# Kernel tuning notes

Measured on AMD Instinct MI355X. Metric: run time of the kernel, lower is better.

Reference implementation:

```python
import jax, jax.numpy as jnp
import numpy as np

GAMMA = 0.95  # usage decay from NTM.__init__

def setup_inputs() -> dict:
    key = jax.random.key(0)
    ks = jax.random.split(key, 16)
    B, N, M, R, U, Din = 256, 32768, 64, 4, 256, 512
    Dc = Din + R * M  # controller input = x concat prev read vectors
    s = 0.02
    x = jax.random.normal(ks[0], (B, Din), jnp.float32)
    A = jax.random.normal(ks[1], (N, M), jnp.float32) * 0.1
    wr_prev = jax.nn.softmax(jax.random.normal(ks[2], (R, B, N), jnp.float32), axis=-1)
    wu_prev = jax.random.uniform(ks[3], (B, N), jnp.float32)
    read_prev = jax.random.normal(ks[4], (R, B, M), jnp.float32) * 0.1
    h = jax.random.normal(ks[5], (B, U), jnp.float32) * 0.1
    c = jax.random.normal(ks[6], (B, U), jnp.float32) * 0.1
    W = jax.random.normal(ks[7], (Dc, 4 * U), jnp.float32) * s
    Uw = jax.random.normal(ks[8], (U, 4 * U), jnp.float32) * s
    b = jnp.zeros((4 * U,), jnp.float32)
    Wk = jax.random.normal(ks[9], (R, U, M), jnp.float32) * s
    bk = jnp.zeros((R, M), jnp.float32)
    Wa = jax.random.normal(ks[10], (U, R), jnp.float32) * s
    ba = jnp.zeros((R,), jnp.float32)
    return dict(x=x, A=A, wr_prev=wr_prev, wu_prev=wu_prev, read_prev=read_prev,
                h=h, c=c, W=W, Uw=Uw, b=b, Wk=Wk, bk=bk, Wa=Wa, ba=ba)

def reference(x, A, wr_prev, wu_prev, read_prev, h, c, W, Uw, b, Wk, bk, Wa, ba):
    B, N = wu_prev.shape
    R, _, M = read_prev.shape
    # ---- controller (single LSTM cell step, keras gate order i,f,g,o) ----
    ctrl_in = jnp.concatenate([x, read_prev.transpose(1, 0, 2).reshape(B, -1)], axis=-1)
    gates = ctrl_in @ W + h @ Uw + b
    gi, gf, gg, go = jnp.split(gates, 4, axis=-1)
    c_new = jax.nn.sigmoid(gf) * c + jax.nn.sigmoid(gi) * jnp.tanh(gg)
    h_new = jax.nn.sigmoid(go) * jnp.tanh(c_new)  # controller_output [B,U]
    # ---- least-used weights from previous usage ----
    least = jnp.argmin(wu_prev, axis=-1)                       # [B]
    wlu = jax.nn.one_hot(least, N, dtype=wu_prev.dtype)        # [B,N]
    # ---- read heads: cosine-similarity content addressing ----
    kt = jnp.tanh(jnp.einsum('bu,rum->rbm', h_new, Wk) + bk[:, None, :])  # [R,B,M]
    inner = jnp.einsum('rbm,nm->rbn', kt, A)                   # [R,B,N]
    knorm = jnp.linalg.norm(kt, axis=-1)                       # [R,B]
    anorm = jnp.linalg.norm(A, axis=-1)                        # [N]
    Ksim = inner / (knorm[..., None] * anorm[None, None, :] + 1e-16)
    wr = jax.nn.softmax(Ksim, axis=-1)                         # [R,B,N]
    # ---- write head: gated mix of prev read weights and least-used ----
    alpha = jax.nn.sigmoid(jnp.tanh(h_new @ Wa + ba))          # [B,R]
    a = alpha.T[:, :, None]                                    # [R,B,1]
    ww = a * wr_prev + (1.0 - a) * wlu[None]                   # [R,B,N]
    # ---- usage update ----
    wu = GAMMA * wu_prev + jnp.sum(wr + ww, axis=0)            # [B,N]
    # ---- memory: erase least-used row(s), then tanh additive writes ----
    erase = 1.0 - jnp.max(wlu, axis=0)                         # [N]
    A_new = A * erase[:, None]
    for r in range(R):  # small fixed head count
        A_new = jnp.tanh(A_new + jnp.einsum('bn,bm->nm', ww[r], kt[r]))
    # ---- reads and output ----
    reads = jnp.einsum('rbn,nm->rbm', wr, A_new)               # [R,B,M]
    out = jnp.concatenate([h_new, reads.transpose(1, 0, 2).reshape(B, -1)], axis=-1)
    return out
```

## Files before the change

### kernel.cpp

```cpp
#include <hip/hip_runtime.h>
#include <hip/hip_bf16.h>
#include <stdint.h>

#define B_   256
#define N_   32768
#define M_   64
#define R_   4
#define U_   256
#define DIN_ 512
#define DC_  768
#define J4_  1024
#define Q_   1024

__device__ __forceinline__ float sigm(float x){ return 1.f/(1.f+__expf(-x)); }
__device__ __forceinline__ float tanh_f(float x){ float e=__expf(2.f*x); return 1.f - 2.f/(e+1.f); }
__device__ __forceinline__ unsigned short f2bf(float x){
    unsigned u = __float_as_uint(x);
    u += 0x7FFFu + ((u>>16)&1u);
    return (unsigned short)(u>>16);
}
__device__ __forceinline__ float bflo(unsigned u){ return __uint_as_float(u << 16); }
__device__ __forceinline__ float bfhi(unsigned u){ return __uint_as_float(u & 0xFFFF0000u); }

__global__ __launch_bounds__(256) void k_zero(int* lflag, float* l){
    int i = blockIdx.x*256 + threadIdx.x;
    if(i < N_) lflag[i] = 0;
    if(i < Q_) l[i] = 0.f;
}

__global__ __launch_bounds__(256) void k_anorm(const float* A, float* anorm){
    int n = blockIdx.x*4 + (threadIdx.x>>6);
    int lane = threadIdx.x & 63;
    float v = A[n*64 + lane];
    float s = v*v;
    #pragma unroll
    for(int m=1;m<64;m<<=1) s += __shfl_xor(s, m, 64);
    if(lane==0) anorm[n] = sqrtf(s);
}

__global__ __launch_bounds__(256) void k_argmin(const float* wu, int* least, int* lflag){
    __shared__ float sv[256]; __shared__ int si[256];
    int b = blockIdx.x, t = threadIdx.x;
    const float* row = wu + (size_t)b*N_;
    float bv = 3.4e38f; int bi = 0;
    for(int n=t; n<N_; n+=256){ float v = row[n]; if(v < bv){ bv=v; bi=n; } }
    sv[t]=bv; si[t]=bi; __syncthreads();
    for(int s=128;s>0;s>>=1){
        if(t<s){
            float ov=sv[t+s]; int oi=si[t+s];
            if(ov<sv[t] || (ov==sv[t] && oi<si[t])){ sv[t]=ov; si[t]=oi; }
        }
        __syncthreads();
    }
    if(t==0){ least[b]=si[0]; lflag[si[0]]=1; }
}

__global__ __launch_bounds__(256) void k_lstm_gemm(const float* x, const float* rp, const float* h,
                                                   const float* W, const float* Uw, float* gpart){
    __shared__ float s_in[8*128];
    int bt = blockIdx.x >> 3, ks = blockIdx.x & 7;
    int b0 = bt*8, t = threadIdx.x;
    for(int i=t; i<1024; i+=256){
        int bb = i>>7, kk = i&127, k = ks*128 + kk, b = b0+bb;
        float v;
        if(k < DIN_) v = x[b*DIN_ + k];
        else if(k < DC_){ int k2 = k - DIN_; v = rp[(k2>>6)*(B_*M_) + b*M_ + (k2&63)]; }
        else v = h[b*U_ + (k-DC_)];
        s_in[bb*128 + kk] = v;
    }
    __syncthreads();
    float4 acc[8];
    #pragma unroll
    for(int i=0;i<8;i++) acc[i] = make_float4(0.f,0.f,0.f,0.f);
    const float* Wsel; int krel;
    if(ks < 6){ Wsel = W; krel = ks*128; } else { Wsel = Uw; krel = ks*128 - DC_; }
    int j0 = t*4;
    for(int kk=0; kk<128; kk++){
        float4 w = *(const float4*)(Wsel + (size_t)(krel+kk)*J4_ + j0);
        #pragma unroll
        for(int bb=0;bb<8;bb++){
            float s = s_in[bb*128 + kk];
            acc[bb].x += s*w.x; acc[bb].y += s*w.y; acc[bb].z += s*w.z; acc[bb].w += s*w.w;
        }
    }
    #pragma unroll
    for(int bb=0;bb<8;bb++)
        *(float4*)(gpart + (size_t)ks*(B_*J4_) + (size_t)(b0+bb)*J4_ + j0) = acc[bb];
}

__global__ __launch_bounds__(256) void k_lstm_act(const float* gpart, const float* bias, const float* c,
                                                  float* h_new, float* out){
    int b = blockIdx.x, u = threadIdx.x;
    float gi=bias[u], gf=bias[256+u], gg=bias[512+u], go=bias[768+u];
    #pragma unroll
    for(int s=0;s<8;s++){
        const float* gp = gpart + (size_t)s*(B_*J4_) + (size_t)b*J4_;
        gi += gp[u]; gf += gp[256+u]; gg += gp[512+u]; go += gp[768+u];
    }
    float cn = sigm(gf)*c[b*U_+u] + sigm(gi)*tanh_f(gg);
    float hn = sigm(go)*tanh_f(cn);
    h_new[b*U_+u] = hn;
    out[(size_t)b*512 + u] = hn;
}

__global__ __launch_bounds__(64) void k_kta(const float* h_new, const float* Wk, const float* bk,
                                            const float* Wa, const float* ba,
                                            float* kt, float* aktw, float* alpha, float* knorm){
    __shared__ float h_l[256];
    int r = blockIdx.x >> 8, b = blockIdx.x & 255, m = threadIdx.x;
    for(int i=m;i<256;i+=64) h_l[i] = h_new[b*U_ + i];
    __syncthreads();
    float acc = bk[r*64 + m];
    const float* wkp = Wk + (size_t)r*U_*M_ + m;
    for(int u=0;u<256;u++) acc += h_l[u] * wkp[u*64];
    float k = tanh_f(acc);
    float s = k*k;
    #pragma unroll
    for(int mm=1;mm<64;mm<<=1) s += __shfl_xor(s, mm, 64);
    float pa = 0.f;
    #pragma unroll
    for(int uu=0; uu<4; uu++){ int u = m*4+uu; pa += h_l[u]*Wa[u*R_ + r]; }
    #pragma unroll
    for(int mm=1;mm<64;mm<<=1) pa += __shfl_xor(pa, mm, 64);
    float al = sigm(tanh_f(pa + ba[r]));
    int q = r*256 + b;
    kt[q*64 + m]   = k;
    aktw[q*64 + m] = al*k;
    if(m==0){ knorm[q] = sqrtf(s); alpha[q] = al; }
}

__global__ __launch_bounds__(256,2) void k_Ggemm(const float* wrp, const float* aktw, float* G){
    __shared__ float wr_l[32*256];
    __shared__ float akt_l[32*64];
    int r = blockIdx.x >> 7, nt = blockIdx.x & 127;
    int nb = nt*256, t = threadIdx.x;
    int tm = t & 15, tn = t >> 4;
    const float* wbase = wrp  + (size_t)r*((size_t)B_*N_);
    const float* abase = aktw + (size_t)r*(B_*M_);
    float4 acc[16];
    #pragma unroll
    for(int i=0;i<16;i++) acc[i]=make_float4(0.f,0.f,0.f,0.f);
    for(int tile=0; tile<8; tile++){
        int bb0 = tile*32;
        __syncthreads();
        for(int i=t; i<2048; i+=256){
            int kk = i>>6, cc = i&63;
            *(float4*)(wr_l + kk*256 + cc*4) = *(const float4*)(wbase + (size_t)(bb0+kk)*N_ + nb + cc*4);
        }
        for(int i=t; i<512; i+=256){
            int kk = i>>4, cc = i&15;
            *(float4*)(akt_l + kk*64 + cc*4) = *(const float4*)(abase + (bb0+kk)*64 + cc*4);
        }
        __syncthreads();
        #pragma unroll 4
        for(int kk=0; kk<32; kk++){
            float4 af = *(const float4*)(akt_l + kk*64 + tm*4);
            float4 w0 = *(const float4*)(wr_l + kk*256 + tn*16);
            float4 w1 = *(const float4*)(wr_l + kk*256 + tn*16 + 4);
            float4 w2 = *(const float4*)(wr_l + kk*256 + tn*16 + 8);
            float4 w3 = *(const float4*)(wr_l + kk*256 + tn*16 + 12);
#define GFMA(I, WV) { acc[I].x += (WV)*af.x; acc[I].y += (WV)*af.y; acc[I].z += (WV)*af.z; acc[I].w += (WV)*af.w; }
            GFMA(0,w0.x) GFMA(1,w0.y) GFMA(2,w0.z) GFMA(3,w0.w)
            GFMA(4,w1.x) GFMA(5,w1.y) GFMA(6,w1.z) GFMA(7,w1.w)
            GFMA(8,w2.x) GFMA(9,w2.y) GFMA(10,w2.z) GFMA(11,w2.w)
            GFMA(12,w3.x) GFMA(13,w3.y) GFMA(14,w3.z) GFMA(15,w3.w)
#undef GFMA
        }
    }
    float* gout = G + (size_t)r*((size_t)N_*64);
    #pragma unroll
    for(int i=0;i<16;i++)
        *(float4*)(gout + (size_t)(nb + tn*16 + i)*64 + tm*4) = acc[i];
}

__global__ __launch_bounds__(64) void k_scatter(const float* kt, const float* alpha, const int* least, float* G){
    int r = blockIdx.x >> 8, b = blockIdx.x & 255, m = threadIdx.x;
    int q = r*256+b;
    float v = (1.f - alpha[q]) * kt[q*64 + m];
    int row = least[b];
    atomicAdd(G + (size_t)r*((size_t)N_*64) + (size_t)row*64 + m, v);
}

__global__ __launch_bounds__(256) void k_Aupd(const float* A, const float* G, const int* lflag, float* Anew){
    int i4 = blockIdx.x*256 + threadIdx.x;
    int n = i4 >> 4;
    float er = lflag[n] ? 0.f : 1.f;
    float4 a = ((const float4*)A)[i4];
    float4 v = make_float4(a.x*er, a.y*er, a.z*er, a.w*er);
    #pragma unroll
    for(int r=0;r<4;r++){
        float4 g = ((const float4*)G)[(size_t)r*524288 + i4];
        v.x = tanh_f(v.x+g.x); v.y = tanh_f(v.y+g.y); v.z = tanh_f(v.z+g.z); v.w = tanh_f(v.w+g.w);
    }
    ((float4*)Anew)[i4] = v;
}

__global__ __launch_bounds__(256,2) void k_scores(const float* kt, const float* A,
                                                  const float* knorm, const float* anorm,
                                                  unsigned short* Pt, float* l){
    __shared__ float4 kt_l[128*16];
    __shared__ float4 A_l[128*16];
    int nt = blockIdx.x >> 3, qt = blockIdx.x & 7;
    int nb = nt*128, qb = qt*128;
    int t = threadIdx.x, tq = t & 15, tn = t >> 4;
    for(int i=t;i<2048;i+=256){
        int row = i>>4, cc = i&15;
        kt_l[row*16 + (cc ^ (row>>3))] = *(const float4*)(kt + (qb+row)*64 + cc*4);
        A_l [row*16 + (cc ^ (row>>3))] = *(const float4*)(A + (size_t)(nb+row)*64 + cc*4);
    }
    __syncthreads();
    float acc[64];
    #pragma unroll
    for(int i=0;i<64;i++) acc[i]=0.f;
    #pragma unroll
    for(int mq=0; mq<16; mq++){
        float4 kf[8], af[8];
        #pragma unroll
        for(int i=0;i<8;i++) kf[i] = kt_l[(tq*8+i)*16 + (mq ^ tq)];
        #pragma unroll
        for(int j=0;j<8;j++) af[j] = A_l[(tn*8+j)*16 + (mq ^ tn)];
        #pragma unroll
        for(int i=0;i<8;i++)
        #pragma unroll
        for(int j=0;j<8;j++)
            acc[i*8+j] += kf[i].x*af[j].x + kf[i].y*af[j].y + kf[i].z*af[j].z + kf[i].w*af[j].w;
    }
    float kn[8], an[8];
    #pragma unroll
    for(int i=0;i<8;i++) kn[i] = knorm[qb + tq*8 + i];
    #pragma unroll
    for(int j=0;j<8;j++) an[j] = anorm[nb + tn*8 + j];
    float lp[8];
    #pragma unroll
    for(int i=0;i<8;i++) lp[i]=0.f;
    #pragma unroll
    for(int j=0;j<8;j++){
        unsigned pk[4];
        #pragma unroll
        for(int i2=0;i2<4;i2++){
            float p0 = __expf(__fdividef(acc[(i2*2  )*8+j], kn[i2*2  ]*an[j] + 1e-16f));
            float p1 = __expf(__fdividef(acc[(i2*2+1)*8+j], kn[i2*2+1]*an[j] + 1e-16f));
            lp[i2*2] += p0; lp[i2*2+1] += p1;
            pk[i2] = (unsigned)f2bf(p0) | ((unsigned)f2bf(p1)<<16);
        }
        *(uint4*)(Pt + (size_t)(nb + tn*8 + j)*Q_ + qb + tq*8) = make_uint4(pk[0],pk[1],pk[2],pk[3]);
    }
    __syncthreads();
    float* lred = (float*)A_l;
    #pragma unroll
    for(int i=0;i<8;i++) lred[tn*128 + tq*8 + i] = lp[i];
    __syncthreads();
    if(t < 128){
        float s = 0.f;
        #pragma unroll
        for(int g=0; g<16; g++) s += lred[g*128 + t];
        atomicAdd(l + qb + t, s);
    }
}

__global__ __launch_bounds__(256,4) void k_pv(const unsigned short* Pt, const float* Anew, float* part){
    __shared__ uint4  P_l[32*16];
    __shared__ float4 V_l[32*16];
    int ch = blockIdx.x >> 3, qt = blockIdx.x & 7;
    int qb = qt*128, n0c = ch*512;
    int t = threadIdx.x, tq = t & 15, tm = t >> 4;
    float4 acc[8];
    #pragma unroll
    for(int i=0;i<8;i++) acc[i]=make_float4(0.f,0.f,0.f,0.f);
    for(int tile=0; tile<16; tile++){
        int n0 = n0c + tile*32;
        __syncthreads();
        for(int i=t;i<512;i+=256){
            int row = i>>4, cc = i&15;
            P_l[row*16 + cc] = *(const uint4*)(Pt + (size_t)(n0+row)*Q_ + qb + cc*8);
            V_l[row*16 + cc] = *(const float4*)(Anew + (size_t)(n0+row)*64 + cc*4);
        }
        __syncthreads();
        #pragma unroll 4
        for(int kk=0;kk<32;kk++){
            uint4 pw = P_l[kk*16 + tq];
            float4 vf = V_l[kk*16 + tm];
            float p0=bflo(pw.x), p1=bfhi(pw.x), p2=bflo(pw.y), p3=bfhi(pw.y);
            float p4=bflo(pw.z), p5=bfhi(pw.z), p6=bflo(pw.w), p7=bfhi(pw.w);
#define PVF(I, PV) { acc[I].x += (PV)*vf.x; acc[I].y += (PV)*vf.y; acc[I].z += (PV)*vf.z; acc[I].w += (PV)*vf.w; }
            PVF(0,p0) PVF(1,p1) PVF(2,p2) PVF(3,p3) PVF(4,p4) PVF(5,p5) PVF(6,p6) PVF(7,p7)
#undef PVF
        }
    }
    #pragma unroll
    for(int i=0;i<8;i++)
        *(float4*)(part + (size_t)ch*(Q_*64) + (size_t)(qb + tq*8 + i)*64 + tm*4) = acc[i];
}

__global__ __launch_bounds__(256) void k_reduce(const float* part, const float* l, float* out){
    int tg = blockIdx.x*256 + threadIdx.x;
    int q = tg >> 6, m = tg & 63;
    float s = 0.f;
    for(int cc=0;cc<64;cc++) s += part[(size_t)cc*(Q_*64) + tg];
    float val = s / l[q];
    int r = q >> 8, b = q & 255;
    out[(size_t)b*512 + 256 + r*64 + m] = val;
}

extern "C" void kernel_launch(void* const* d_in, const int* in_sizes, int n_in,
                              void* d_out, int out_size, void* d_ws, size_t ws_size,
                              hipStream_t stream) {
    const float* x        = (const float*)d_in[0];
    const float* A        = (const float*)d_in[1];
    const float* wr_prev  = (const float*)d_in[2];
    const float* wu_prev  = (const float*)d_in[3];
    const float* read_prev= (const float*)d_in[4];
    const float* h        = (const float*)d_in[5];
    const float* c        = (const float*)d_in[6];
    const float* W        = (const float*)d_in[7];
    const float* Uw       = (const float*)d_in[8];
    const float* bvec     = (const float*)d_in[9];
    const float* Wk       = (const float*)d_in[10];
    const float* bk       = (const float*)d_in[11];
    const float* Wa       = (const float*)d_in[12];
    const float* ba       = (const float*)d_in[13];
    float* out = (float*)d_out;

    char* wsp = (char*)d_ws;
    float* G      = (float*)(wsp);
    float* Anew   = (float*)(wsp + 33554432);
    unsigned short* Pt = (unsigned short*)(wsp + 41943040);
    float* h_new  = (float*)(wsp + 109051904);
    float* kt     = (float*)(wsp + 109314048);
    float* aktw   = (float*)(wsp + 109576192);
    float* alpha  = (float*)(wsp + 109838336);
    float* knorm  = (float*)(wsp + 109842432);
    float* anorm  = (float*)(wsp + 109846528);
    int*   lflag  = (int*)  (wsp + 109977600);
    float* l      = (float*)(wsp + 110108672);
    int*   least  = (int*)  (wsp + 110112768);

    k_zero     <<<128, 256, 0, stream>>>(lflag, l);
    k_anorm    <<<8192,256, 0, stream>>>(A, anorm);
    k_argmin   <<<256, 256, 0, stream>>>(wu_prev, least, lflag);
    k_lstm_gemm<<<256, 256, 0, stream>>>(x, read_prev, h, W, Uw, G);
    k_lstm_act <<<256, 256, 0, stream>>>(G, bvec, c, h_new, out);
    k_kta      <<<1024, 64, 0, stream>>>(h_new, Wk, bk, Wa, ba, kt, aktw, alpha, knorm);
    k_Ggemm    <<<512, 256, 0, stream>>>(wr_prev, aktw, G);
    k_scatter  <<<1024, 64, 0, stream>>>(kt, alpha, least, G);
    k_Aupd     <<<2048,256, 0, stream>>>(A, G, lflag, Anew);
    k_scores   <<<2048,256, 0, stream>>>(kt, A, knorm, anorm, Pt, l);
    k_pv       <<<512, 256, 0, stream>>>(Pt, Anew, G);
    k_reduce   <<<256, 256, 0, stream>>>(G, l, out);
}
```

Before: 558.2 us.

## Fuse scores and PV into flash-style bf16 MFMA attention kernel

Result: faster. 494.9 us (-11.3%).

```diff
diff --git a/kernel.cpp b/kernel.cpp
--- a/kernel.cpp
+++ b/kernel.cpp
@@ -11,6 +11,10 @@
 #define DC_  768
 #define J4_  1024
 #define Q_   1024
+#define NPART_ 32
+
+typedef __attribute__((ext_vector_type(8))) short short8v;
+typedef __attribute__((ext_vector_type(4))) float f32x4;
 
 __device__ __forceinline__ float sigm(float x){ return 1.f/(1.f+__expf(-x)); }
 __device__ __forceinline__ float tanh_f(float x){ float e=__expf(2.f*x); return 1.f - 2.f/(e+1.f); }
@@ -19,8 +23,6 @@
     u += 0x7FFFu + ((u>>16)&1u);
     return (unsigned short)(u>>16);
 }
-__device__ __forceinline__ float bflo(unsigned u){ return __uint_as_float(u << 16); }
-__device__ __forceinline__ float bfhi(unsigned u){ return __uint_as_float(u & 0xFFFF0000u); }
 
 __global__ __launch_bounds__(256) void k_zero(int* lflag, float* l){
     int i = blockIdx.x*256 + threadIdx.x;
@@ -28,10 +30,11 @@
     if(i < Q_) l[i] = 0.f;
 }
 
-__global__ __launch_bounds__(256) void k_anorm(const float* A, float* anorm){
+__global__ __launch_bounds__(256) void k_anorm(const float* A, float* anorm, unsigned short* A_bf){
     int n = blockIdx.x*4 + (threadIdx.x>>6);
     int lane = threadIdx.x & 63;
     float v = A[n*64 + lane];
+    A_bf[n*64 + lane] = f2bf(v);
     float s = v*v;
     #pragma unroll
     for(int m=1;m<64;m<<=1) s += __shfl_xor(s, m, 64);
@@ -105,7 +108,8 @@
 
 __global__ __launch_bounds__(64) void k_kta(const float* h_new, const float* Wk, const float* bk,
                                             const float* Wa, const float* ba,
-                                            float* kt, float* aktw, float* alpha, float* knorm){
+                                            float* kt, unsigned short* kt_bf, float* aktw,
+                                            float* alpha, float* knorm){
     __shared__ float h_l[256];
     int r = blockIdx.x >> 8, b = blockIdx.x & 255, m = threadIdx.x;
     for(int i=m;i<256;i+=64) h_l[i] = h_new[b*U_ + i];
@@ -124,8 +128,9 @@
     for(int mm=1;mm<64;mm<<=1) pa += __shfl_xor(pa, mm, 64);
     float al = sigm(tanh_f(pa + ba[r]));
     int q = r*256 + b;
-    kt[q*64 + m]   = k;
-    aktw[q*64 + m] = al*k;
+    kt[q*64 + m]    = k;
+    kt_bf[q*64 + m] = f2bf(k);
+    aktw[q*64 + m]  = al*k;
     if(m==0){ knorm[q] = sqrtf(s); alpha[q] = al; }
 }
 
@@ -195,108 +200,107 @@
     ((float4*)Anew)[i4] = v;
 }
 
-__global__ __launch_bounds__(256,2) void k_scores(const float* kt, const float* A,
-                                                  const float* knorm, const float* anorm,
-                                                  unsigned short* Pt, float* l){
-    __shared__ float4 kt_l[128*16];
-    __shared__ float4 A_l[128*16];
-    int nt = blockIdx.x >> 3, qt = blockIdx.x & 7;
-    int nb = nt*128, qb = qt*128;
-    int t = threadIdx.x, tq = t & 15, tn = t >> 4;
-    for(int i=t;i<2048;i+=256){
-        int row = i>>4, cc = i&15;
-        kt_l[row*16 + (cc ^ (row>>3))] = *(const float4*)(kt + (qb+row)*64 + cc*4);
-        A_l [row*16 + (cc ^ (row>>3))] = *(const float4*)(A + (size_t)(nb+row)*64 + cc*4);
+__global__ __launch_bounds__(256) void k_vt(const float* Anew, unsigned short* Vt){
+    __shared__ __align__(16) unsigned short lt[4096];
+    int n0 = blockIdx.x*64, t = threadIdx.x;
+    int row = t>>2, cb = t&3;
+    #pragma unroll
+    for(int i=0;i<4;i++){
+        int cidx = cb*4 + i;
+        float4 f = *(const float4*)(Anew + (size_t)(n0+row)*64 + cidx*4);
+        int m0 = cidx*4;
+        lt[(m0  )*64 + row] = f2bf(f.x);
+        lt[(m0+1)*64 + row] = f2bf(f.y);
+        lt[(m0+2)*64 + row] = f2bf(f.z);
+        lt[(m0+3)*64 + row] = f2bf(f.w);
     }
     __syncthreads();
-    float acc[64];
-    #pragma unroll
-    for(int i=0;i<64;i++) acc[i]=0.f;
-    #pragma unroll
-    for(int mq=0; mq<16; mq++){
-        float4 kf[8], af[8];
+    int mr = t>>2;
+    #pragma unroll
+    for(int cc=0; cc<2; cc++){
+        int c = (t&3) + cc*4;
+        uint4 v = *(const uint4*)(lt + mr*64 + c*8);
+        *(uint4*)(Vt + (size_t)mr*N_ + n0 + c*8) = v;
+    }
+}
+
+__global__ __launch_bounds__(256) void k_attn(const unsigned short* kt_bf, const unsigned short* A_bf,
+                                              const unsigned short* Vt, const float* knorm,
+                                              const float* anorm, float* part, float* l){
+    __shared__ __align__(16) unsigned short Pl[64*256];
+    int nc = blockIdx.x >> 4, qt = blockIdx.x & 15;
+    int qb = qt*64, nb = nc*1024;
+    int lane = threadIdx.x & 63, w = threadIdx.x >> 6;
+    int r16 = lane & 15, hq = lane >> 4;
+    const short8v* kp = (const short8v*)(kt_bf + (size_t)(qb + w*16 + r16)*64 + hq*8);
+    short8v ka0 = kp[0], ka1 = kp[4];
+    float kn[4];
+    #pragma unroll
+    for(int j=0;j<4;j++) kn[j] = knorm[qb + w*16 + hq*4 + j];
+    f32x4 O[4];
+    #pragma unroll
+    for(int mt=0;mt<4;mt++) O[mt] = (f32x4){0.f,0.f,0.f,0.f};
+    float lp[4] = {0.f,0.f,0.f,0.f};
+    int g2 = (r16 >> 2) & 3;
+
+    for(int c=0; c<4; c++){
+        int n0c = nb + c*256;
+        __syncthreads();
+        for(int nt=0; nt<16; nt++){
+            int ntb = n0c + nt*16;
+            const short8v* bp = (const short8v*)(A_bf + (size_t)(ntb + r16)*64 + hq*8);
+            f32x4 acc = (f32x4){0.f,0.f,0.f,0.f};
+            acc = __builtin_amdgcn_mfma_f32_16x16x32_bf16(ka0, bp[0], acc, 0, 0, 0);
+            acc = __builtin_amdgcn_mfma_f32_16x16x32_bf16(ka1, bp[4], acc, 0, 0, 0);
+            float an = anorm[ntb + r16];
+            unsigned um[4];
+            #pragma unroll
+            for(int j=0;j<4;j++){
+                float p = __expf(__fdividef(acc[j], kn[j]*an + 1e-16f));
+                lp[j] += p;
+                um[j] = (unsigned)f2bf(p);
+            }
+            int nl = nt*16 + (r16 & ~1);
+            #pragma unroll
+            for(int j=0;j<4;j++){
+                unsigned up = __shfl_xor((int)um[j], 1, 64);
+                if((lane & 1) == 0){
+                    unsigned word = um[j] | (up << 16);
+                    int byteoff = (w*16 + hq*4 + j)*512 + ((nl ^ (hq<<4)) << 1);
+                    *(unsigned*)((char*)Pl + byteoff) = word;
+                }
+            }
+        }
+        __syncthreads();
+        #pragma unroll 2
+        for(int ks=0; ks<8; ks++){
+            short8v pa = *(const short8v*)((const char*)Pl +
+                          ((w*16 + r16)*512 + (((ks*32 + hq*8) ^ (g2<<4)) << 1)));
+            #pragma unroll
+            for(int mt=0; mt<4; mt++){
+                const short8v* vp = (const short8v*)(Vt + (size_t)(mt*16 + r16)*N_ + n0c + ks*32 + hq*8);
+                O[mt] = __builtin_amdgcn_mfma_f32_16x16x32_bf16(pa, vp[0], O[mt], 0, 0, 0);
+            }
+        }
+    }
+    #pragma unroll
+    for(int mt=0; mt<4; mt++)
         #pragma unroll
-        for(int i=0;i<8;i++) kf[i] = kt_l[(tq*8+i)*16 + (mq ^ tq)];
+        for(int j=0;j<4;j++)
+            part[((size_t)nc*Q_ + (qb + w*16 + hq*4 + j))*64 + mt*16 + r16] = O[mt][j];
+    #pragma unroll
+    for(int j=0;j<4;j++){
         #pragma unroll
-        for(int j=0;j<8;j++) af[j] = A_l[(tn*8+j)*16 + (mq ^ tn)];
-        #pragma unroll
-        for(int i=0;i<8;i++)
-        #pragma unroll
-        for(int j=0;j<8;j++)
-            acc[i*8+j] += kf[i].x*af[j].x + kf[i].y*af[j].y + kf[i].z*af[j].z + kf[i].w*af[j].w;
-    }
-    float kn[8], an[8];
-    #pragma unroll
-    for(int i=0;i<8;i++) kn[i] = knorm[qb + tq*8 + i];
-    #pragma unroll
-    for(int j=0;j<8;j++) an[j] = anorm[nb + tn*8 + j];
-    float lp[8];
-    #pragma unroll
-    for(int i=0;i<8;i++) lp[i]=0.f;
-    #pragma unroll
-    for(int j=0;j<8;j++){
-        unsigned pk[4];
-        #pragma unroll
-        for(int i2=0;i2<4;i2++){
-            float p0 = __expf(__fdividef(acc[(i2*2  )*8+j], kn[i2*2  ]*an[j] + 1e-16f));
-            float p1 = __expf(__fdividef(acc[(i2*2+1)*8+j], kn[i2*2+1]*an[j] + 1e-16f));
-            lp[i2*2] += p0; lp[i2*2+1] += p1;
-            pk[i2] = (unsigned)f2bf(p0) | ((unsigned)f2bf(p1)<<16);
-        }
-        *(uint4*)(Pt + (size_t)(nb + tn*8 + j)*Q_ + qb + tq*8) = make_uint4(pk[0],pk[1],pk[2],pk[3]);
-    }
-    __syncthreads();
-    float* lred = (float*)A_l;
-    #pragma unroll
-    for(int i=0;i<8;i++) lred[tn*128 + tq*8 + i] = lp[i];
-    __syncthreads();
-    if(t < 128){
-        float s = 0.f;
-        #pragma unroll
-        for(int g=0; g<16; g++) s += lred[g*128 + t];
-        atomicAdd(l + qb + t, s);
-    }
-}
-
-__global__ __launch_bounds__(256,4) void k_pv(const unsigned short* Pt, const float* Anew, float* part){
-    __shared__ uint4  P_l[32*16];
-    __shared__ float4 V_l[32*16];
-    int ch = blockIdx.x >> 3, qt = blockIdx.x & 7;
-    int qb = qt*128, n0c = ch*512;
-    int t = threadIdx.x, tq = t & 15, tm = t >> 4;
-    float4 acc[8];
-    #pragma unroll
-    for(int i=0;i<8;i++) acc[i]=make_float4(0.f,0.f,0.f,0.f);
-    for(int tile=0; tile<16; tile++){
-        int n0 = n0c + tile*32;
-        __syncthreads();
-        for(int i=t;i<512;i+=256){
-            int row = i>>4, cc = i&15;
-            P_l[row*16 + cc] = *(const uint4*)(Pt + (size_t)(n0+row)*Q_ + qb + cc*8);
-            V_l[row*16 + cc] = *(const float4*)(Anew + (size_t)(n0+row)*64 + cc*4);
-        }
-        __syncthreads();
-        #pragma unroll 4
-        for(int kk=0;kk<32;kk++){
-            uint4 pw = P_l[kk*16 + tq];
-            float4 vf = V_l[kk*16 + tm];
-            float p0=bflo(pw.x), p1=bfhi(pw.x), p2=bflo(pw.y), p3=bfhi(pw.y);
-            float p4=bflo(pw.z), p5=bfhi(pw.z), p6=bflo(pw.w), p7=bfhi(pw.w);
-#define PVF(I, PV) { acc[I].x += (PV)*vf.x; acc[I].y += (PV)*vf.y; acc[I].z += (PV)*vf.z; acc[I].w += (PV)*vf.w; }
-            PVF(0,p0) PVF(1,p1) PVF(2,p2) PVF(3,p3) PVF(4,p4) PVF(5,p5) PVF(6,p6) PVF(7,p7)
-#undef PVF
-        }
-    }
-    #pragma unroll
-    for(int i=0;i<8;i++)
-        *(float4*)(part + (size_t)ch*(Q_*64) + (size_t)(qb + tq*8 + i)*64 + tm*4) = acc[i];
+        for(int m2=1;m2<16;m2<<=1) lp[j] += __shfl_xor(lp[j], m2, 64);
+        if(r16 == 0) atomicAdd(l + qb + w*16 + hq*4 + j, lp[j]);
+    }
 }
 
 __global__ __launch_bounds__(256) void k_reduce(const float* part, const float* l, float* out){
     int tg = blockIdx.x*256 + threadIdx.x;
     int q = tg >> 6, m = tg & 63;
     float s = 0.f;
-    for(int cc=0;cc<64;cc++) s += part[(size_t)cc*(Q_*64) + tg];
+    for(int cc=0;cc<NPART_;cc++) s += part[(size_t)cc*(Q_*64) + tg];
     float val = s / l[q];
     int r = q >> 8, b = q & 255;
     out[(size_t)b*512 + 256 + r*64 + m] = val;
@@ -324,27 +328,30 @@
     char* wsp = (char*)d_ws;
     float* G      = (float*)(wsp);
     float* Anew   = (float*)(wsp + 33554432);
-    unsigned short* Pt = (unsigned short*)(wsp + 41943040);
-    float* h_new  = (float*)(wsp + 109051904);
-    float* kt     = (float*)(wsp + 109314048);
-    float* aktw   = (float*)(wsp + 109576192);
-    float* alpha  = (float*)(wsp + 109838336);
-    float* knorm  = (float*)(wsp + 109842432);
-    float* anorm  = (float*)(wsp + 109846528);
-    int*   lflag  = (int*)  (wsp + 109977600);
-    float* l      = (float*)(wsp + 110108672);
-    int*   least  = (int*)  (wsp + 110112768);
+    float* part   = (float*)(wsp + 41943040);
+    unsigned short* A_bf  = (unsigned short*)(wsp + 50331648);
+    unsigned short* Vt_bf = (unsigned short*)(wsp + 54525952);
+    unsigned short* kt_bf = (unsigned short*)(wsp + 58720256);
+    float* h_new  = (float*)(wsp + 58851328);
+    float* kt     = (float*)(wsp + 59113472);
+    float* aktw   = (float*)(wsp + 59375616);
+    float* alpha  = (float*)(wsp + 59637760);
+    float* knorm  = (float*)(wsp + 59641856);
+    float* anorm  = (float*)(wsp + 59645952);
+    int*   lflag  = (int*)  (wsp + 59777024);
+    float* l      = (float*)(wsp + 59908096);
+    int*   least  = (int*)  (wsp + 59912192);
 
     k_zero     <<<128, 256, 0, stream>>>(lflag, l);
-    k_anorm    <<<8192,256, 0, stream>>>(A, anorm);
+    k_anorm    <<<8192,256, 0, stream>>>(A, anorm, A_bf);
     k_argmin   <<<256, 256, 0, stream>>>(wu_prev, least, lflag);
     k_lstm_gemm<<<256, 256, 0, stream>>>(x, read_prev, h, W, Uw, G);
     k_lstm_act <<<256, 256, 0, stream>>>(G, bvec, c, h_new, out);
-    k_kta      <<<1024, 64, 0, stream>>>(h_new, Wk, bk, Wa, ba, kt, aktw, alpha, knorm);
+    k_kta      <<<1024, 64, 0, stream>>>(h_new, Wk, bk, Wa, ba, kt, kt_bf, aktw, alpha, knorm);
     k_Ggemm    <<<512, 256, 0, stream>>>(wr_prev, aktw, G);
     k_scatter  <<<1024, 64, 0, stream>>>(kt, alpha, least, G);
     k_Aupd     <<<2048,256, 0, stream>>>(A, G, lflag, Anew);
-    k_scores   <<<2048,256, 0, stream>>>(kt, A, knorm, anorm, Pt, l);
-    k_pv       <<<512, 256, 0, stream>>>(Pt, Anew, G);
-    k_reduce   <<<256, 256, 0, stream>>>(G, l, out);
-}
+    k_vt       <<<512, 256, 0, stream>>>(Anew, Vt_bf);
+    k_attn     <<<512, 256, 0, stream>>>(kt_bf, A_bf, Vt_bf, knorm, anorm, part, l);
+    k_reduce   <<<256, 256, 0, stream>>>(part, l, out);
+}
```
